# Kernel tuning notes

Measured on AMD Instinct MI355X. Metric: run time of the kernel, lower is better.

Reference implementation:

```python
import jax, jax.numpy as jnp
import numpy as np

HIDDEN = 512
HEAD = 64
SEQ = 2048
CHUNK = 256
GAMMA = 0.96875
SCALE_BASE = 512.0


def _xpos(x, downscale):
    # x: [B, L, hd]; XPOS with offset=0 (scale rows == length, no trimming needed)
    B, L, hd = x.shape
    half = hd // 2
    scale_vec = (jnp.arange(0, hd, 2, dtype=jnp.float32) + 0.4 * hd) / (1.4 * hd)  # [half]
    power = jnp.arange(L, dtype=jnp.float32) / SCALE_BASE                          # [L]
    scale = scale_vec[None, :] ** power[:, None]                                   # [L, half]
    inv_freq = 1.0 / (10000.0 ** (jnp.arange(half, dtype=jnp.float32) / half))
    sinusoid = jnp.arange(L, dtype=jnp.float32)[:, None] * inv_freq[None, :]       # [L, half]
    sin, cos = jnp.sin(sinusoid), jnp.cos(sinusoid)
    if downscale:
        scale = 1.0 / scale
    # duplicate_interleave: repeat each column twice -> [L, hd]
    sin_f = jnp.repeat(sin * scale, 2, axis=-1)
    cos_f = jnp.repeat(cos * scale, 2, axis=-1)
    x1 = x[:, :, 0::2]
    x2 = x[:, :, 1::2]
    rot = jnp.stack((-x2, x1), axis=-1).reshape(B, L, hd)  # rotate_every_two
    return x * cos_f + rot * sin_f


def _D_parallel():
    # D[i, j] = gamma^|i-j| if j < (i//chunk + 1)*chunk else 0 (block-causal with in-chunk lookahead)
    i = jnp.arange(SEQ)[:, None]
    j = jnp.arange(SEQ)[None, :]
    j_max = (i // CHUNK + 1) * CHUNK
    decay = GAMMA ** jnp.abs(i - j).astype(jnp.float32)
    return jnp.where(j < j_max, decay, 0.0)  # gamma>0 so no NaNs to scrub


def setup_inputs() -> dict:
    key = jax.random.key(0)
    k1, k2, k3, k4 = jax.random.split(key, 4)
    X = jax.random.normal(k1, (8, SEQ, HIDDEN), dtype=jnp.float32)
    W_Q = jax.random.normal(k2, (HIDDEN, HEAD), dtype=jnp.float32) / HIDDEN
    W_K = jax.random.normal(k3, (HIDDEN, HEAD), dtype=jnp.float32) / HIDDEN
    W_V = jax.random.normal(k4, (HIDDEN, HEAD), dtype=jnp.float32) / HIDDEN
    return {"X": X, "W_Q": W_Q, "W_K": W_K, "W_V": W_V}


def reference(X, W_Q, W_K, W_V):
    Q = _xpos(X @ W_Q, downscale=False)   # [B, S, H]
    K = _xpos(X @ W_K, downscale=True)    # [B, S, H]
    V = X @ W_V                           # [B, S, V]
    D = _D_parallel()                     # [S, S]
    scores = jnp.einsum('bqh,bkh->bqk', Q, K) * D[None]
    return jnp.einsum('bqk,bkv->bqv', scores, V)
```

## Files before the change

### kernel.cpp

```cpp
#include <hip/hip_runtime.h>
#include <hip/hip_bf16.h>


typedef __attribute__((ext_vector_type(8))) short short8;
typedef __attribute__((ext_vector_type(4))) float floatx4;

#define LOG2GAMMA (-0.04580350f)

static __device__ __forceinline__ unsigned short f2bf(float f) {
    __hip_bfloat16 h = __float2bfloat16(f);
    return *reinterpret_cast<unsigned short*>(&h);
}

__global__ __launch_bounds__(256) void prep_kernel(
    const float* __restrict__ Wq, const float* __restrict__ Wk,
    const float* __restrict__ Wv,
    __hip_bfloat16* __restrict__ Wt, float* __restrict__ tabs)
{
    int idx = blockIdx.x * 256 + threadIdx.x;
    const int WT_N = 192 * 512;
    if (idx < WT_N) {
        int n = idx >> 9, k = idx & 511;
        int m = n >> 6, c = n & 63;
        const float* W = (m == 0) ? Wq : ((m == 1) ? Wk : Wv);
        Wt[idx] = __float2bfloat16(W[k * 64 + c]);
    } else {
        int t2 = idx - WT_N;
        if (t2 < 4 * 2048 * 32) {
            int tab = t2 >> 16;
            int rem = t2 & 65535;
            int pos = rem >> 5;
            int t   = rem & 31;
            float inv_freq = powf(10000.0f, -(float)t / 32.0f);
            float sinus = (float)pos * inv_freq;
            float s = sinf(sinus), c = cosf(sinus);
            float sv = (2.0f * (float)t + 0.4f * 64.0f) / (1.4f * 64.0f);
            float power = (float)pos / 512.0f;
            float scl = powf(sv, (tab >= 2) ? -power : power);
            tabs[t2] = ((tab & 1) == 0) ? c * scl : s * scl;
        }
    }
}

__global__ __launch_bounds__(256) void proj_kernel(
    const float* __restrict__ X, const __hip_bfloat16* __restrict__ Wt,
    const float* __restrict__ tabs,
    __hip_bfloat16* __restrict__ Qb, __hip_bfloat16* __restrict__ Kb,
    __hip_bfloat16* __restrict__ Vt)
{
    __shared__ __hip_bfloat16 lx[64][136];
    __shared__ __hip_bfloat16 lw[192][136];

    int tid = threadIdx.x;
    int r0 = blockIdx.x * 64;
    int w = tid >> 6, lane = tid & 63, quad = lane >> 4, l15 = lane & 15;

    floatx4 acc[12];
#pragma unroll
    for (int t = 0; t < 12; t++) acc[t] = (floatx4){0.f, 0.f, 0.f, 0.f};

    for (int kb = 0; kb < 4; kb++) {
#pragma unroll
        for (int u = 0; u < 8; u++) {
            int f = u * 256 + tid;
            int row = f >> 5, c = f & 31;
            float4 v = *(const float4*)(X + (r0 + row) * 512 + kb * 128 + c * 4);
            ushort4 pk;
            pk.x = f2bf(v.x); pk.y = f2bf(v.y); pk.z = f2bf(v.z); pk.w = f2bf(v.w);
            *(ushort4*)&lx[row][c * 4] = pk;
        }
#pragma unroll
        for (int u = 0; u < 12; u++) {
            int f = u * 256 + tid;
            int row = f >> 4, c = f & 15;
            uint4 v = *(const uint4*)(Wt + row * 512 + kb * 128 + c * 8);
            *(uint4*)&lw[row][c * 8] = v;
        }
        __syncthreads();
#pragma unroll
        for (int ks = 0; ks < 4; ks++) {
            short8 a = *(const short8*)&lx[w * 16 + l15][ks * 32 + quad * 8];
#pragma unroll
            for (int t = 0; t < 12; t++) {
                short8 bfr = *(const short8*)&lw[t * 16 + l15][ks * 32 + quad * 8];
                acc[t] = __builtin_amdgcn_mfma_f32_16x16x32_bf16(a, bfr, acc[t], 0, 0, 0);
            }
        }
        __syncthreads();
    }

    int rbase = r0 + w * 16 + quad * 4;
#pragma unroll
    for (int rg = 0; rg < 4; rg++) {
        int r = rbase + rg;
        int b = r >> 11, n = r & 2047;
#pragma unroll
        for (int t = 0; t < 4; t++) {
            float val = acc[t][rg];
            float prt = __shfl_xor(val, 1, 64);
            int ch = t * 16 + l15;
            int tt = ch >> 1;
            float co = tabs[n * 32 + tt];
            float si = tabs[65536 + n * 32 + tt];
            float o = (l15 & 1) ? (val * co + prt * si) : (val * co - prt * si);
            Qb[(b * 2048 + n) * 64 + ch] = __float2bfloat16(o);
        }
#pragma unroll
        for (int t = 4; t < 8; t++) {
            float val = acc[t][rg];
            float prt = __shfl_xor(val, 1, 64);
            int ch = (t - 4) * 16 + l15;
            int tt = ch >> 1;
            float co = tabs[131072 + n * 32 + tt];
            float si = tabs[196608 + n * 32 + tt];
            float o = (l15 & 1) ? (val * co + prt * si) : (val * co - prt * si);
            Kb[(b * 2048 + n) * 64 + ch] = __float2bfloat16(o);
        }
#pragma unroll
        for (int t = 8; t < 12; t++) {
            int ch = (t - 8) * 16 + l15;
            Vt[(b * 64 + ch) * 2048 + n] = __float2bfloat16(acc[t][rg]);
        }
    }
}

__global__ __launch_bounds__(256) void attn_kernel(
    const __hip_bfloat16* __restrict__ Qb, const __hip_bfloat16* __restrict__ Kb,
    const __hip_bfloat16* __restrict__ Vt, float* __restrict__ out)
{
    __shared__ __hip_bfloat16 lk[256][72];
    __shared__ __hip_bfloat16 lv[64][264];
    __shared__ __hip_bfloat16 lp[4][16][264];

    int tid = threadIdx.x;
    int b = blockIdx.x >> 5, qsub = blockIdx.x & 31;
    int q0 = qsub * 64, qc = qsub >> 2;
    int w = tid >> 6, lane = tid & 63, quad = lane >> 4, l15 = lane & 15;

    short8 qf[2];
#pragma unroll
    for (int kk = 0; kk < 2; kk++)
        qf[kk] = *(const short8*)(Qb + (b * 2048 + q0 + w * 16 + l15) * 64 + kk * 32 + quad * 8);

    floatx4 o[4];
#pragma unroll
    for (int t = 0; t < 4; t++) o[t] = (floatx4){0.f, 0.f, 0.f, 0.f};

    int kc0 = (qc >= 3) ? (qc - 3) : 0;
    for (int kc = kc0; kc <= qc; kc++) {
        int kbase = kc * 256;
#pragma unroll
        for (int u = 0; u < 8; u++) {
            int f = u * 256 + tid;
            int row = f >> 3, c = f & 7;
            *(uint4*)&lk[row][c * 8] =
                *(const uint4*)(Kb + (b * 2048 + kbase + row) * 64 + c * 8);
        }
#pragma unroll
        for (int u = 0; u < 8; u++) {
            int f = u * 256 + tid;
            int row = f >> 5, c = f & 31;
            *(uint4*)&lv[row][c * 8] =
                *(const uint4*)(Vt + (b * 64 + row) * 2048 + kbase + c * 8);
        }
        __syncthreads();

        floatx4 s[16];
#pragma unroll
        for (int t = 0; t < 16; t++) s[t] = (floatx4){0.f, 0.f, 0.f, 0.f};
#pragma unroll
        for (int t = 0; t < 16; t++) {
#pragma unroll
            for (int kk = 0; kk < 2; kk++) {
                short8 bfr = *(const short8*)&lk[t * 16 + l15][kk * 32 + quad * 8];
                s[t] = __builtin_amdgcn_mfma_f32_16x16x32_bf16(qf[kk], bfr, s[t], 0, 0, 0);
            }
        }

        int i0 = q0 + w * 16 + quad * 4;
#pragma unroll
        for (int t = 0; t < 16; t++) {
            int j = kbase + t * 16 + l15;
#pragma unroll
            for (int rg = 0; rg < 4; rg++) {
                int d = i0 + rg - j; d = (d < 0) ? -d : d;
                float p = s[t][rg] * exp2f(LOG2GAMMA * (float)d);
                lp[w][quad * 4 + rg][t * 16 + l15] = __float2bfloat16(p);
            }
        }
        __syncthreads();

#pragma unroll
        for (int ks = 0; ks < 8; ks++) {
            short8 a = *(const short8*)&lp[w][l15][ks * 32 + quad * 8];
#pragma unroll
            for (int t2 = 0; t2 < 4; t2++) {
                short8 bfr = *(const short8*)&lv[t2 * 16 + l15][ks * 32 + quad * 8];
                o[t2] = __builtin_amdgcn_mfma_f32_16x16x32_bf16(a, bfr, o[t2], 0, 0, 0);
            }
        }
        __syncthreads();
    }

    int rbase = b * 2048 + q0 + w * 16 + quad * 4;
#pragma unroll
    for (int t2 = 0; t2 < 4; t2++)
#pragma unroll
        for (int rg = 0; rg < 4; rg++)
            out[(rbase + rg) * 64 + t2 * 16 + l15] = o[t2][rg];
}

extern "C" void kernel_launch(void* const* d_in, const int* in_sizes, int n_in,
                              void* d_out, int out_size, void* d_ws, size_t ws_size,
                              hipStream_t stream) {
    const float* X  = (const float*)d_in[0];
    const float* Wq = (const float*)d_in[1];
    const float* Wk = (const float*)d_in[2];
    const float* Wv = (const float*)d_in[3];
    float* out = (float*)d_out;

    char* ws = (char*)d_ws;
    __hip_bfloat16* Wt   = (__hip_bfloat16*)(ws);
    float*          tabs = (float*)(ws + 196608);
    __hip_bfloat16* Qb   = (__hip_bfloat16*)(ws + 1245184);
    __hip_bfloat16* Kb   = (__hip_bfloat16*)(ws + 3342336);
    __hip_bfloat16* Vt   = (__hip_bfloat16*)(ws + 5439488);

    prep_kernel<<<1408, 256, 0, stream>>>(Wq, Wk, Wv, Wt, tabs);
    proj_kernel<<<256, 256, 0, stream>>>(X, Wt, tabs, Qb, Kb, Vt);
    attn_kernel<<<256, 256, 0, stream>>>(Qb, Kb, Vt, out);
}
```

Baseline: 128.0 us.

## Halve row tiles in proj and attn kernels, split N across waves, read V directly

Both the projection and attention kernels now process 32 rows per block instead of 64 and launch 512 blocks, with waves splitting output columns (and key subtiles) so 256 CUs are better filled. The projection stages V through LDS so it can be written to the transposed Vt layout with coalesced 16-byte stores. The attention kernel drops the LDS copy of V and reads V fragments directly from global memory in the PV MFMA loop, which removes one barrier and adds launch_bounds occupancy hints. The cost is more redundant K loads per block and uncached global V reads inside the inner loop.

```diff
diff --git a/kernel.cpp b/kernel.cpp
--- a/kernel.cpp
+++ b/kernel.cpp
@@ -42,26 +42,27 @@
     }
 }
 
-__global__ __launch_bounds__(256) void proj_kernel(
+__global__ __launch_bounds__(256, 2) void proj_kernel(
     const float* __restrict__ X, const __hip_bfloat16* __restrict__ Wt,
     const float* __restrict__ tabs,
     __hip_bfloat16* __restrict__ Qb, __hip_bfloat16* __restrict__ Kb,
     __hip_bfloat16* __restrict__ Vt)
 {
-    __shared__ __hip_bfloat16 lx[64][136];
+    __shared__ __hip_bfloat16 lx[32][136];
     __shared__ __hip_bfloat16 lw[192][136];
 
     int tid = threadIdx.x;
-    int r0 = blockIdx.x * 64;
+    int r0 = blockIdx.x * 32;
     int w = tid >> 6, lane = tid & 63, quad = lane >> 4, l15 = lane & 15;
-
-    floatx4 acc[12];
-#pragma unroll
-    for (int t = 0; t < 12; t++) acc[t] = (floatx4){0.f, 0.f, 0.f, 0.f};
+    int rh = w & 1, nh = w >> 1;
+
+    floatx4 acc[6];
+#pragma unroll
+    for (int t = 0; t < 6; t++) acc[t] = (floatx4){0.f, 0.f, 0.f, 0.f};
 
     for (int kb = 0; kb < 4; kb++) {
 #pragma unroll
-        for (int u = 0; u < 8; u++) {
+        for (int u = 0; u < 4; u++) {
             int f = u * 256 + tid;
             int row = f >> 5, c = f & 31;
             float4 v = *(const float4*)(X + (r0 + row) * 512 + kb * 128 + c * 4);
@@ -79,72 +80,89 @@
         __syncthreads();
 #pragma unroll
         for (int ks = 0; ks < 4; ks++) {
-            short8 a = *(const short8*)&lx[w * 16 + l15][ks * 32 + quad * 8];
-#pragma unroll
-            for (int t = 0; t < 12; t++) {
-                short8 bfr = *(const short8*)&lw[t * 16 + l15][ks * 32 + quad * 8];
+            short8 a = *(const short8*)&lx[rh * 16 + l15][ks * 32 + quad * 8];
+#pragma unroll
+            for (int t = 0; t < 6; t++) {
+                short8 bfr = *(const short8*)&lw[(nh * 6 + t) * 16 + l15][ks * 32 + quad * 8];
                 acc[t] = __builtin_amdgcn_mfma_f32_16x16x32_bf16(a, bfr, acc[t], 0, 0, 0);
             }
         }
         __syncthreads();
     }
 
-    int rbase = r0 + w * 16 + quad * 4;
-#pragma unroll
-    for (int rg = 0; rg < 4; rg++) {
-        int r = rbase + rg;
-        int b = r >> 11, n = r & 2047;
-#pragma unroll
-        for (int t = 0; t < 4; t++) {
-            float val = acc[t][rg];
+    int b0 = r0 >> 11, n0 = r0 & 2047;
+    int rbase = r0 + rh * 16 + quad * 4;
+
+    __hip_bfloat16* lvt = &lx[0][0];
+    if (nh == 1) {
+#pragma unroll
+        for (int tl = 2; tl < 6; tl++) {
+            int ch = (tl - 2) * 16 + l15;
+#pragma unroll
+            for (int rg = 0; rg < 4; rg++)
+                lvt[ch * 40 + rh * 16 + quad * 4 + rg] = __float2bfloat16(acc[tl][rg]);
+        }
+    }
+    __syncthreads();
+
+#pragma unroll
+    for (int tl = 0; tl < 6; tl++) {
+        int t = nh * 6 + tl;
+        if (t >= 8) break;
+#pragma unroll
+        for (int rg = 0; rg < 4; rg++) {
+            int r = rbase + rg;
+            int b = r >> 11, n = r & 2047;
+            float val = acc[tl][rg];
             float prt = __shfl_xor(val, 1, 64);
-            int ch = t * 16 + l15;
-            int tt = ch >> 1;
-            float co = tabs[n * 32 + tt];
-            float si = tabs[65536 + n * 32 + tt];
-            float o = (l15 & 1) ? (val * co + prt * si) : (val * co - prt * si);
-            Qb[(b * 2048 + n) * 64 + ch] = __float2bfloat16(o);
-        }
-#pragma unroll
-        for (int t = 4; t < 8; t++) {
-            float val = acc[t][rg];
-            float prt = __shfl_xor(val, 1, 64);
-            int ch = (t - 4) * 16 + l15;
-            int tt = ch >> 1;
-            float co = tabs[131072 + n * 32 + tt];
-            float si = tabs[196608 + n * 32 + tt];
-            float o = (l15 & 1) ? (val * co + prt * si) : (val * co - prt * si);
-            Kb[(b * 2048 + n) * 64 + ch] = __float2bfloat16(o);
-        }
-#pragma unroll
-        for (int t = 8; t < 12; t++) {
-            int ch = (t - 8) * 16 + l15;
-            Vt[(b * 64 + ch) * 2048 + n] = __float2bfloat16(acc[t][rg]);
-        }
-    }
-}
-
-__global__ __launch_bounds__(256) void attn_kernel(
+            if (t < 4) {
+                int ch = t * 16 + l15;
+                int tt = ch >> 1;
+                float co = tabs[n * 32 + tt];
+                float si = tabs[65536 + n * 32 + tt];
+                float o = (l15 & 1) ? (val * co + prt * si) : (val * co - prt * si);
+                Qb[(b * 2048 + n) * 64 + ch] = __float2bfloat16(o);
+            } else {
+                int ch = (t - 4) * 16 + l15;
+                int tt = ch >> 1;
+                float co = tabs[131072 + n * 32 + tt];
+                float si = tabs[196608 + n * 32 + tt];
+                float o = (l15 & 1) ? (val * co + prt * si) : (val * co - prt * si);
+                Kb[(b * 2048 + n) * 64 + ch] = __float2bfloat16(o);
+            }
+        }
+    }
+
+    {
+        int row = tid >> 2, c = tid & 3;
+        uint4 v = *(const uint4*)&lvt[row * 40 + c * 8];
+        *(uint4*)(Vt + ((size_t)(b0 * 64 + row)) * 2048 + n0 + c * 8) = v;
+    }
+}
+
+__global__ __launch_bounds__(256, 3) void attn_kernel(
     const __hip_bfloat16* __restrict__ Qb, const __hip_bfloat16* __restrict__ Kb,
     const __hip_bfloat16* __restrict__ Vt, float* __restrict__ out)
 {
     __shared__ __hip_bfloat16 lk[256][72];
-    __shared__ __hip_bfloat16 lv[64][264];
-    __shared__ __hip_bfloat16 lp[4][16][264];
+    __shared__ __hip_bfloat16 lp[32][264];
 
     int tid = threadIdx.x;
-    int b = blockIdx.x >> 5, qsub = blockIdx.x & 31;
-    int q0 = qsub * 64, qc = qsub >> 2;
+    int b = blockIdx.x >> 6, qt = blockIdx.x & 63;
+    int q0 = qt * 32, qc = q0 >> 8;
     int w = tid >> 6, lane = tid & 63, quad = lane >> 4, l15 = lane & 15;
+    int rh = w & 1, ph = w >> 1;
 
     short8 qf[2];
 #pragma unroll
     for (int kk = 0; kk < 2; kk++)
-        qf[kk] = *(const short8*)(Qb + (b * 2048 + q0 + w * 16 + l15) * 64 + kk * 32 + quad * 8);
-
-    floatx4 o[4];
-#pragma unroll
-    for (int t = 0; t < 4; t++) o[t] = (floatx4){0.f, 0.f, 0.f, 0.f};
+        qf[kk] = *(const short8*)(Qb + ((size_t)(b * 2048 + q0 + rh * 16 + l15)) * 64 + kk * 32 + quad * 8);
+
+    const __hip_bfloat16* vbase = Vt + (size_t)b * 64 * 2048;
+
+    floatx4 o[2];
+    o[0] = (floatx4){0.f, 0.f, 0.f, 0.f};
+    o[1] = (floatx4){0.f, 0.f, 0.f, 0.f};
 
     int kc0 = (qc >= 3) ? (qc - 3) : 0;
     for (int kc = kc0; kc <= qc; kc++) {
@@ -154,60 +172,54 @@
             int f = u * 256 + tid;
             int row = f >> 3, c = f & 7;
             *(uint4*)&lk[row][c * 8] =
-                *(const uint4*)(Kb + (b * 2048 + kbase + row) * 64 + c * 8);
-        }
-#pragma unroll
-        for (int u = 0; u < 8; u++) {
-            int f = u * 256 + tid;
-            int row = f >> 5, c = f & 31;
-            *(uint4*)&lv[row][c * 8] =
-                *(const uint4*)(Vt + (b * 64 + row) * 2048 + kbase + c * 8);
-        }
-        __syncthreads();
-
-        floatx4 s[16];
-#pragma unroll
-        for (int t = 0; t < 16; t++) s[t] = (floatx4){0.f, 0.f, 0.f, 0.f};
-#pragma unroll
-        for (int t = 0; t < 16; t++) {
+                *(const uint4*)(Kb + ((size_t)(b * 2048 + kbase + row)) * 64 + c * 8);
+        }
+        __syncthreads();
+
+        floatx4 s[8];
+#pragma unroll
+        for (int t = 0; t < 8; t++) s[t] = (floatx4){0.f, 0.f, 0.f, 0.f};
+#pragma unroll
+        for (int t = 0; t < 8; t++) {
 #pragma unroll
             for (int kk = 0; kk < 2; kk++) {
-                short8 bfr = *(const short8*)&lk[t * 16 + l15][kk * 32 + quad * 8];
+                short8 bfr = *(const short8*)&lk[(ph * 8 + t) * 16 + l15][kk * 32 + quad * 8];
                 s[t] = __builtin_amdgcn_mfma_f32_16x16x32_bf16(qf[kk], bfr, s[t], 0, 0, 0);
             }
         }
 
-        int i0 = q0 + w * 16 + quad * 4;
-#pragma unroll
-        for (int t = 0; t < 16; t++) {
-            int j = kbase + t * 16 + l15;
+        int i0 = q0 + rh * 16 + quad * 4;
+#pragma unroll
+        for (int t = 0; t < 8; t++) {
+            int j = kbase + (ph * 8 + t) * 16 + l15;
 #pragma unroll
             for (int rg = 0; rg < 4; rg++) {
                 int d = i0 + rg - j; d = (d < 0) ? -d : d;
                 float p = s[t][rg] * exp2f(LOG2GAMMA * (float)d);
-                lp[w][quad * 4 + rg][t * 16 + l15] = __float2bfloat16(p);
+                lp[rh * 16 + quad * 4 + rg][(ph * 8 + t) * 16 + l15] = __float2bfloat16(p);
             }
         }
         __syncthreads();
 
 #pragma unroll
         for (int ks = 0; ks < 8; ks++) {
-            short8 a = *(const short8*)&lp[w][l15][ks * 32 + quad * 8];
-#pragma unroll
-            for (int t2 = 0; t2 < 4; t2++) {
-                short8 bfr = *(const short8*)&lv[t2 * 16 + l15][ks * 32 + quad * 8];
-                o[t2] = __builtin_amdgcn_mfma_f32_16x16x32_bf16(a, bfr, o[t2], 0, 0, 0);
-            }
-        }
-        __syncthreads();
-    }
-
-    int rbase = b * 2048 + q0 + w * 16 + quad * 4;
-#pragma unroll
-    for (int t2 = 0; t2 < 4; t2++)
+            short8 a = *(const short8*)&lp[rh * 16 + l15][ks * 32 + quad * 8];
+#pragma unroll
+            for (int tt = 0; tt < 2; tt++) {
+                int t2 = ph * 2 + tt;
+                short8 bfr = *(const short8*)(vbase + ((size_t)(t2 * 16 + l15)) * 2048
+                                              + kbase + ks * 32 + quad * 8);
+                o[tt] = __builtin_amdgcn_mfma_f32_16x16x32_bf16(a, bfr, o[tt], 0, 0, 0);
+            }
+        }
+    }
+
+    int rbase = b * 2048 + q0 + rh * 16 + quad * 4;
+#pragma unroll
+    for (int tt = 0; tt < 2; tt++)
 #pragma unroll
         for (int rg = 0; rg < 4; rg++)
-            out[(rbase + rg) * 64 + t2 * 16 + l15] = o[t2][rg];
+            out[((size_t)(rbase + rg)) * 64 + (ph * 2 + tt) * 16 + l15] = o[tt][rg];
 }
 
 extern "C" void kernel_launch(void* const* d_in, const int* in_sizes, int n_in,
@@ -227,6 +239,6 @@
     __hip_bfloat16* Vt   = (__hip_bfloat16*)(ws + 5439488);
 
     prep_kernel<<<1408, 256, 0, stream>>>(Wq, Wk, Wv, Wt, tabs);
-    proj_kernel<<<256, 256, 0, stream>>>(X, Wt, tabs, Qb, Kb, Vt);
-    attn_kernel<<<256, 256, 0, stream>>>(Qb, Kb, Vt, out);
-}
+    proj_kernel<<<512, 256, 0, stream>>>(X, Wt, tabs, Qb, Kb, Vt);
+    attn_kernel<<<512, 256, 0, stream>>>(Qb, Kb, Vt, out);
+}
```

Measured after the change: 125.7 us. About the same (-1.8%).
